# Kernel optimization log

Hardware: AMD Instinct MI355X
Metric: run time of the kernel (lower is better)

The kernel has to match this reference:

```python
import jax, jax.numpy as jnp
import numpy as np

B, S, E, H = 16, 512, 768, 12
D = E // H
SCALING = 1.0 / np.sqrt(D * 1.0)  # scaling_factor = 1


def setup_inputs() -> dict:
    key = jax.random.key(0)
    ks = jax.random.split(key, 8)
    query = jax.random.normal(ks[0], (B, S, E), dtype=jnp.float32)
    key_in = jax.random.normal(ks[1], (B, S, E), dtype=jnp.float32)
    value = jax.random.normal(ks[2], (B, S, E), dtype=jnp.float32)
    key_padding_mask = jax.random.randint(ks[3], (B, S), 0, 2).astype(jnp.bool_)
    attn_bias = jax.random.normal(ks[4], (B, H, S, S), dtype=jnp.float32)
    # Learned params. NOTE: original code applies wq to q, k AND v (wk/wv unused).
    Wq = jax.random.normal(ks[5], (E, E), dtype=jnp.float32) * (1.0 / np.sqrt(E))
    bq = jnp.zeros((E,), dtype=jnp.float32)
    Wo = jax.random.normal(ks[6], (E, E), dtype=jnp.float32) * (1.0 / np.sqrt(E))
    bo = jnp.zeros((E,), dtype=jnp.float32)
    return {"query": query, "key": key_in, "value": value,
            "key_padding_mask": key_padding_mask, "attn_bias": attn_bias,
            "Wq": Wq, "bq": bq, "Wo": Wo, "bo": bo}


def _split_heads(x):
    # [B,S,E] -> [B,H,S,D]
    return x.reshape(B, S, H, D).transpose(0, 2, 1, 3)


def reference(query, key, value, key_padding_mask, attn_bias, Wq, bq, Wo, bo):
    q = (query @ Wq + bq) * jnp.asarray(SCALING, query.dtype)
    k = key @ Wq + bq      # faithful: wq used for k and v in the source
    v = value @ Wq + bq
    q, k, v = _split_heads(q), _split_heads(k), _split_heads(v)  # [B,H,S,D]
    w = jnp.einsum('bhtd,bhsd->bhts', q, k)                      # [B,H,T,S]
    w = jnp.where(key_padding_mask[:, None, None, :], -jnp.inf, w)
    w = w + attn_bias
    attn = jax.nn.softmax(w, axis=-1)  # dropout is no-op (training=False)
    o = jnp.einsum('bhts,bhsd->bhtd', attn, v)
    o = o.transpose(0, 2, 1, 3).reshape(B, S, E)
    o = o @ Wo + bo
    attn_weights = w.reshape(B * H, S, S)
    return (o, attn_weights, attn.reshape(B * H, S, S))
```

## Files before the change

### kernel.cpp

```cpp
#include <hip/hip_runtime.h>
#include <cmath>

#define BB 16
#define SS 512
#define EE 768
#define HH 12
#define DD 64
#define NBH (BB*HH)

#define MASK_NEG (-1.0e30f)

__device__ __forceinline__ unsigned short bf16_rn(float x) {
    unsigned u = __float_as_uint(x);
    u += 0x7FFFu + ((u >> 16) & 1u);
    return (unsigned short)(u >> 16);
}
__device__ __forceinline__ float bf16_tof(unsigned short h) {
    return __uint_as_float(((unsigned)h) << 16);
}

typedef __attribute__((ext_vector_type(8))) short bf16x8;
typedef __attribute__((ext_vector_type(4))) float f32x4;
typedef __attribute__((ext_vector_type(4))) unsigned short u16x4;

__global__ __launch_bounds__(256) void conv_w_kernel(
    const float* __restrict__ Wq, const float* __restrict__ Wo,
    unsigned short* __restrict__ wtq, unsigned short* __restrict__ wto)
{
    const float* __restrict__ W = blockIdx.z ? Wo : Wq;
    unsigned short* __restrict__ wt = blockIdx.z ? wto : wtq;
    const int k = blockIdx.x * 256 + threadIdx.x;
    const int n = blockIdx.y;
    const float x = W[(size_t)k * EE + n];
    const unsigned short h = bf16_rn(x);
    const float r = x - bf16_tof(h);
    const unsigned short m = bf16_rn(r);
    const float l2 = r - bf16_tof(m);
    const unsigned short l = bf16_rn(l2);
    const size_t PL = (size_t)EE * EE;
    wt[0 * PL + (size_t)n * EE + k] = h;
    wt[1 * PL + (size_t)n * EE + k] = m;
    wt[2 * PL + (size_t)n * EE + k] = l;
}

__global__ __launch_bounds__(256) void split_gemm_qkv_kernel(
    const float* __restrict__ Xq, const float* __restrict__ Xk,
    const float* __restrict__ Xv, const unsigned short* __restrict__ wt,
    const float* __restrict__ bvec,
    unsigned short* __restrict__ qp, unsigned short* __restrict__ kp,
    unsigned short* __restrict__ vtp)
{
    const int p = blockIdx.x;
    const int z = p / 384;
    const int q = p % 384;
    const int xcd = q & 7, idx = q >> 3;
    const int m0 = (xcd * 8 + (idx & 7)) * 128;
    const int n0 = (idx >> 3) * 128;

    const float* __restrict__ X = (z == 1) ? Xk : (z == 2) ? Xv : Xq;
    const float scale = (z == 0) ? 0.125f : 1.0f;

    __shared__ __align__(16) unsigned short lds[4 * 4096];
    const int AH = 0, AL = 4096, BH = 8192, BL = 12288;

    const int tid = threadIdx.x;
    const int srow = tid >> 2;
    const int sg   = tid & 3;
    const int wv = tid >> 6;
    const int wr = wv >> 1, wc = wv & 1;
    const int lane = tid & 63;
    const int l15 = lane & 15, lg = lane >> 4;

    const size_t PL = (size_t)EE * EE;
    const size_t PS = (size_t)NBH * SS * DD;

    f32x4 acc[4][4];
#pragma unroll
    for (int i = 0; i < 4; ++i)
#pragma unroll
        for (int j = 0; j < 4; ++j) acc[i][j] = (f32x4){0.f, 0.f, 0.f, 0.f};

    float4 xf[2][2];
    bf16x8 wh[2], wl[2];

#define QKV_LOAD(K0)                                                          \
    {                                                                         \
        _Pragma("unroll")                                                     \
        for (int half = 0; half < 2; ++half) {                                \
            const int row = srow + 64 * half;                                 \
            const float* xp = &X[(size_t)(m0 + row) * EE + (K0) + sg * 8];    \
            xf[half][0] = *reinterpret_cast<const float4*>(xp);               \
            xf[half][1] = *reinterpret_cast<const float4*>(xp + 4);           \
            const size_t bo = (size_t)(n0 + row) * EE + (K0) + sg * 8;        \
            wh[half] = *reinterpret_cast<const bf16x8*>(&wt[0 * PL + bo]);    \
            wl[half] = *reinterpret_cast<const bf16x8*>(&wt[1 * PL + bo]);    \
        }                                                                     \
    }

    QKV_LOAD(0);

#pragma unroll 1
    for (int k0 = 0; k0 < EE; k0 += 32) {
        __syncthreads();
#pragma unroll
        for (int half = 0; half < 2; ++half) {
            const int row = srow + 64 * half;
            const float xs[8] = {xf[half][0].x, xf[half][0].y, xf[half][0].z, xf[half][0].w,
                                 xf[half][1].x, xf[half][1].y, xf[half][1].z, xf[half][1].w};
            bf16x8 hv, mv;
#pragma unroll
            for (int e = 0; e < 8; ++e) {
                const float x = xs[e];
                const unsigned short h = bf16_rn(x);
                const unsigned short m = bf16_rn(x - bf16_tof(h));
                hv[e] = (short)h;
                mv[e] = (short)m;
            }
            const int o = row * 32 + sg * 8;
            *reinterpret_cast<bf16x8*>(&lds[AH + o]) = hv;
            *reinterpret_cast<bf16x8*>(&lds[AL + o]) = mv;
            *reinterpret_cast<bf16x8*>(&lds[BH + o]) = wh[half];
            *reinterpret_cast<bf16x8*>(&lds[BL + o]) = wl[half];
        }
        __syncthreads();

        if (k0 + 32 < EE) QKV_LOAD(k0 + 32);

        bf16x8 ah[4], al[4];
#pragma unroll
        for (int i = 0; i < 4; ++i) {
            const int o = (wr * 64 + i * 16 + l15) * 32 + lg * 8;
            ah[i] = *reinterpret_cast<const bf16x8*>(&lds[AH + o]);
            al[i] = *reinterpret_cast<const bf16x8*>(&lds[AL + o]);
        }
#pragma unroll
        for (int j = 0; j < 4; ++j) {
            const int o = (wc * 64 + j * 16 + l15) * 32 + lg * 8;
            const bf16x8 bh = *reinterpret_cast<const bf16x8*>(&lds[BH + o]);
            const bf16x8 bl = *reinterpret_cast<const bf16x8*>(&lds[BL + o]);
#pragma unroll
            for (int i = 0; i < 4; ++i) {
                acc[i][j] = __builtin_amdgcn_mfma_f32_16x16x32_bf16(ah[i], bh, acc[i][j], 0, 0, 0);
                acc[i][j] = __builtin_amdgcn_mfma_f32_16x16x32_bf16(ah[i], bl, acc[i][j], 0, 0, 0);
                acc[i][j] = __builtin_amdgcn_mfma_f32_16x16x32_bf16(al[i], bh, acc[i][j], 0, 0, 0);
                acc[i][j] = __builtin_amdgcn_mfma_f32_16x16x32_bf16(al[i], bl, acc[i][j], 0, 0, 0);
            }
        }
    }
#undef QKV_LOAD

    unsigned short* __restrict__ dstp = (z == 0) ? qp : kp;
#pragma unroll
    for (int j = 0; j < 4; ++j) {
        const int n = n0 + wc * 64 + j * 16 + l15;
        const float bvn = bvec[n];
        const int h = n >> 6, d = n & 63;
#pragma unroll
        for (int i = 0; i < 4; ++i) {
            const int mb = m0 + wr * 64 + i * 16 + lg * 4;
#pragma unroll
            for (int r = 0; r < 4; ++r) {
                const int m = mb + r;
                const int bh_ = (m >> 9) * HH + h;
                const int srow_ = m & 511;
                const float val = (acc[i][j][r] + bvn) * scale;
                const unsigned short hi = bf16_rn(val);
                const unsigned short lo = bf16_rn(val - bf16_tof(hi));
                if (z == 2) {
                    const size_t o = ((size_t)bh_ * DD + d) * SS + srow_;
                    vtp[o] = hi;
                    vtp[o + PS] = lo;
                } else {
                    const size_t o = ((size_t)bh_ * SS + srow_) * DD + d;
                    dstp[o] = hi;
                    dstp[o + PS] = lo;
                }
            }
        }
    }
}

__global__ __launch_bounds__(256) void flash_attn_kernel(
    const unsigned short* __restrict__ qp, const unsigned short* __restrict__ kp,
    const unsigned short* __restrict__ vt, const unsigned char* __restrict__ mask,
    const float* __restrict__ bias, float* __restrict__ wout,
    float* __restrict__ ohb, float* __restrict__ stat_m,
    float* __restrict__ stat_inv)
{
    const int p = blockIdx.x;
    const int g = p >> 3;
    const int bh = (p & 7) * 24 + (g >> 3);
    const int t0 = (g & 7) * 64;
    const int b = bh / HH, h = bh % HH;
    const int tid = threadIdx.x;
    const int wv = tid >> 6;
    const int lane = tid & 63, l15 = lane & 15, lg = lane >> 4;
    const size_t PS = (size_t)NBH * SS * DD;

    __shared__ __align__(16) unsigned short kbuf[2 * 64 * 68];
    __shared__ __align__(16) unsigned short vbuf[2 * 64 * 68];
    __shared__ __align__(16) unsigned short pbuf[4 * 2 * 16 * 68];

    bf16x8 bqh[2], bql[2];
    {
        const unsigned short* qbase = &qp[((size_t)bh * SS + t0 + wv * 16) * DD];
#pragma unroll
        for (int kc = 0; kc < 2; ++kc) {
            const size_t o = (size_t)l15 * DD + kc * 32 + lg * 8;
            bqh[kc] = *reinterpret_cast<const bf16x8*>(&qbase[o]);
            bql[kc] = *reinterpret_cast<const bf16x8*>(&qbase[o + PS]);
        }
    }

    float rm = -3.0e38f, rs = 0.0f;

    f32x4 oac[4];
#pragma unroll
    for (int j = 0; j < 4; ++j) oac[j] = (f32x4){0.f, 0.f, 0.f, 0.f};

    const int t = t0 + wv * 16 + l15;

    const unsigned short* __restrict__ kb0 = &kp[(size_t)bh * SS * DD];
    const unsigned short* __restrict__ vb0 = &vt[(size_t)bh * DD * SS];
    const int srow2 = tid >> 3, sg2 = (tid & 7) * 8;

    bf16x8 krh[2], krl[2], vrh[2], vrl[2];

#define FA_LOADKV(SC)                                                         \
    {                                                                         \
        _Pragma("unroll")                                                     \
        for (int rep = 0; rep < 2; ++rep) {                                   \
            const int row = srow2 + rep * 32;                                 \
            krh[rep] = *reinterpret_cast<const bf16x8*>(                      \
                &kb0[(size_t)((SC) + row) * DD + sg2]);                       \
            krl[rep] = *reinterpret_cast<const bf16x8*>(                      \
                &kb0[(size_t)((SC) + row) * DD + sg2 + PS]);                  \
            vrh[rep] = *reinterpret_cast<const bf16x8*>(                      \
                &vb0[(size_t)row * SS + (SC) + sg2]);                         \
            vrl[rep] = *reinterpret_cast<const bf16x8*>(                      \
                &vb0[(size_t)row * SS + (SC) + sg2 + PS]);                    \
        }                                                                     \
    }

    FA_LOADKV(0);

#pragma unroll 1
    for (int c = 0; c < 8; ++c) {
        const int sc = c * 64;
        __syncthreads();

#pragma unroll
        for (int rep = 0; rep < 2; ++rep) {
            const int row = srow2 + rep * 32;
            *reinterpret_cast<bf16x8*>(&kbuf[row * 68 + sg2]) = krh[rep];
            *reinterpret_cast<bf16x8*>(&kbuf[64 * 68 + row * 68 + sg2]) = krl[rep];
            *reinterpret_cast<bf16x8*>(&vbuf[row * 68 + sg2]) = vrh[rep];
            *reinterpret_cast<bf16x8*>(&vbuf[64 * 68 + row * 68 + sg2]) = vrl[rep];
        }
        __syncthreads();

        if (c < 7) FA_LOADKV(sc + 64);

        float4 bvr[4];
        uchar4 mkr[4];
#pragma unroll
        for (int i = 0; i < 4; ++i) {
            const int s = sc + i * 16 + lg * 4;
            bvr[i] = *reinterpret_cast<const float4*>(&bias[((size_t)bh * SS + t) * SS + s]);
            mkr[i] = *reinterpret_cast<const uchar4*>(&mask[b * SS + s]);
        }

        f32x4 ws[4];
#pragma unroll
        for (int i = 0; i < 4; ++i) ws[i] = (f32x4){0.f, 0.f, 0.f, 0.f};
#pragma unroll
        for (int kc = 0; kc < 2; ++kc) {
#pragma unroll
            for (int i = 0; i < 4; ++i) {
                const int o = (i * 16 + l15) * 68 + kc * 32 + lg * 8;
                const bf16x8 ah = *reinterpret_cast<const bf16x8*>(&kbuf[o]);
                const bf16x8 al = *reinterpret_cast<const bf16x8*>(&kbuf[64 * 68 + o]);
                ws[i] = __builtin_amdgcn_mfma_f32_16x16x32_bf16(ah, bqh[kc], ws[i], 0, 0, 0);
                ws[i] = __builtin_amdgcn_mfma_f32_16x16x32_bf16(ah, bql[kc], ws[i], 0, 0, 0);
                ws[i] = __builtin_amdgcn_mfma_f32_16x16x32_bf16(al, bqh[kc], ws[i], 0, 0, 0);
                ws[i] = __builtin_amdgcn_mfma_f32_16x16x32_bf16(al, bql[kc], ws[i], 0, 0, 0);
            }
        }

        float mx = -3.0e38f;
#pragma unroll
        for (int i = 0; i < 4; ++i) {
            const int s = sc + i * 16 + lg * 4;
            const size_t go = ((size_t)bh * SS + t) * SS + s;
            float4 w4;
            w4.x = mkr[i].x ? MASK_NEG : ws[i][0] + bvr[i].x;
            w4.y = mkr[i].y ? MASK_NEG : ws[i][1] + bvr[i].y;
            w4.z = mkr[i].z ? MASK_NEG : ws[i][2] + bvr[i].z;
            w4.w = mkr[i].w ? MASK_NEG : ws[i][3] + bvr[i].w;
            *reinterpret_cast<float4*>(&wout[go]) = w4;
            ws[i][0] = w4.x; ws[i][1] = w4.y; ws[i][2] = w4.z; ws[i][3] = w4.w;
            mx = fmaxf(mx, fmaxf(fmaxf(w4.x, w4.y), fmaxf(w4.z, w4.w)));
        }
        mx = fmaxf(mx, __shfl_xor(mx, 16));
        mx = fmaxf(mx, __shfl_xor(mx, 32));

        const float m_new = fmaxf(rm, mx);
        float sm = 0.0f;
#pragma unroll
        for (int i = 0; i < 4; ++i)
#pragma unroll
            for (int r = 0; r < 4; ++r) sm += __expf(ws[i][r] - m_new);
        sm += __shfl_xor(sm, 16);
        sm += __shfl_xor(sm, 32);
        const float scl = __expf(rm - m_new);
        rs = rs * scl + sm;
        rm = m_new;

        unsigned short* pw = &pbuf[(wv * 2) * 16 * 68];
#pragma unroll
        for (int i = 0; i < 4; ++i) {
            float4 p4;
            p4.x = __expf(ws[i][0] - m_new);
            p4.y = __expf(ws[i][1] - m_new);
            p4.z = __expf(ws[i][2] - m_new);
            p4.w = __expf(ws[i][3] - m_new);
            u16x4 hv, lv;
            hv.x = bf16_rn(p4.x); lv.x = bf16_rn(p4.x - bf16_tof(hv.x));
            hv.y = bf16_rn(p4.y); lv.y = bf16_rn(p4.y - bf16_tof(hv.y));
            hv.z = bf16_rn(p4.z); lv.z = bf16_rn(p4.z - bf16_tof(hv.z));
            hv.w = bf16_rn(p4.w); lv.w = bf16_rn(p4.w - bf16_tof(hv.w));
            const int po = l15 * 68 + i * 16 + lg * 4;
            *reinterpret_cast<u16x4*>(&pw[po]) = hv;
            *reinterpret_cast<u16x4*>(&pw[16 * 68 + po]) = lv;
        }

        float sclr[4];
#pragma unroll
        for (int r = 0; r < 4; ++r) sclr[r] = __shfl(scl, lg * 4 + r);
#pragma unroll
        for (int j = 0; j < 4; ++j)
#pragma unroll
            for (int r = 0; r < 4; ++r) oac[j][r] *= sclr[r];

#pragma unroll
        for (int kc = 0; kc < 2; ++kc) {
            const int ko = kc * 32 + lg * 8;
            const bf16x8 pah = *reinterpret_cast<const bf16x8*>(&pw[l15 * 68 + ko]);
            const bf16x8 pal = *reinterpret_cast<const bf16x8*>(&pw[16 * 68 + l15 * 68 + ko]);
#pragma unroll
            for (int j = 0; j < 4; ++j) {
                const int o = (j * 16 + l15) * 68 + ko;
                const bf16x8 vh = *reinterpret_cast<const bf16x8*>(&vbuf[o]);
                const bf16x8 vl = *reinterpret_cast<const bf16x8*>(&vbuf[64 * 68 + o]);
                oac[j] = __builtin_amdgcn_mfma_f32_16x16x32_bf16(pah, vh, oac[j], 0, 0, 0);
                oac[j] = __builtin_amdgcn_mfma_f32_16x16x32_bf16(pah, vl, oac[j], 0, 0, 0);
                oac[j] = __builtin_amdgcn_mfma_f32_16x16x32_bf16(pal, vh, oac[j], 0, 0, 0);
                oac[j] = __builtin_amdgcn_mfma_f32_16x16x32_bf16(pal, vl, oac[j], 0, 0, 0);
            }
        }
    }
#undef FA_LOADKV

    const float inv = 1.0f / rs;
    if (lg == 0) {
        stat_m[(size_t)bh * SS + t] = rm;
        stat_inv[(size_t)bh * SS + t] = inv;
    }
    float invr[4];
#pragma unroll
    for (int r = 0; r < 4; ++r) invr[r] = __shfl(inv, lg * 4 + r);
#pragma unroll
    for (int j = 0; j < 4; ++j)
#pragma unroll
        for (int r = 0; r < 4; ++r) {
            const int tr = t0 + wv * 16 + lg * 4 + r;
            ohb[((size_t)b * SS + tr) * EE + h * DD + j * 16 + l15] = oac[j][r] * invr[r];
        }
}

__global__ __launch_bounds__(256) void finish_kernel(
    const float* __restrict__ X, const unsigned short* __restrict__ wt,
    const float* __restrict__ bvec, float* __restrict__ dflat,
    const float* __restrict__ win, const float* __restrict__ stat_m,
    const float* __restrict__ stat_inv, float* __restrict__ attn)
{
    __shared__ __align__(16) unsigned short lds[6 * 4096];

    if (blockIdx.x >= 384) {
        const int nb = gridDim.x - 384;
        const size_t total = (size_t)NBH * SS * (SS / 4);
        for (size_t g = (size_t)(blockIdx.x - 384) * 256 + threadIdx.x; g < total;
             g += (size_t)nb * 256) {
            const size_t row = g >> 7;
            const float m_ = stat_m[row];
            const float iv = stat_inv[row];
            const float4 w4 = reinterpret_cast<const float4*>(win)[g];
            float4 p4;
            p4.x = __expf(w4.x - m_) * iv;
            p4.y = __expf(w4.y - m_) * iv;
            p4.z = __expf(w4.z - m_) * iv;
            p4.w = __expf(w4.w - m_) * iv;
            reinterpret_cast<float4*>(attn)[g] = p4;
        }
        return;
    }

    const int q = blockIdx.x;
    const int xcd = q & 7, idx = q >> 3;
    const int m0 = (xcd * 8 + (idx & 7)) * 128;
    const int n0 = (idx >> 3) * 128;

    const int AH = 0, AM = 4096, AL = 8192, BH = 12288, BM = 16384, BL = 20480;

    const int tid = threadIdx.x;
    const int srow = tid >> 2;
    const int sg   = tid & 3;
    const int wv = tid >> 6;
    const int wr = wv >> 1, wc = wv & 1;
    const int lane = tid & 63;
    const int l15 = lane & 15, lg = lane >> 4;
    const size_t PL = (size_t)EE * EE;

    f32x4 acc[4][4];
#pragma unroll
    for (int i = 0; i < 4; ++i)
#pragma unroll
        for (int j = 0; j < 4; ++j) acc[i][j] = (f32x4){0.f, 0.f, 0.f, 0.f};

#pragma unroll 1
    for (int k0 = 0; k0 < EE; k0 += 32) {
#pragma unroll
        for (int half = 0; half < 2; ++half) {
            const int row = srow + 64 * half;
            const float* xp = &X[(size_t)(m0 + row) * EE + k0 + sg * 8];
            const float4 f0 = *reinterpret_cast<const float4*>(xp);
            const float4 f1 = *reinterpret_cast<const float4*>(xp + 4);
            const float xs[8] = {f0.x, f0.y, f0.z, f0.w, f1.x, f1.y, f1.z, f1.w};
            bf16x8 hv, mv, lv;
#pragma unroll
            for (int e = 0; e < 8; ++e) {
                const float x = xs[e];
                const unsigned short h = bf16_rn(x);
                const float r = x - bf16_tof(h);
                const unsigned short m = bf16_rn(r);
                const float l2 = r - bf16_tof(m);
                hv[e] = (short)h;
                mv[e] = (short)m;
                lv[e] = (short)bf16_rn(l2);
            }
            const int o = row * 32 + sg * 8;
            *reinterpret_cast<bf16x8*>(&lds[AH + o]) = hv;
            *reinterpret_cast<bf16x8*>(&lds[AM + o]) = mv;
            *reinterpret_cast<bf16x8*>(&lds[AL + o]) = lv;

            const size_t bo = (size_t)(n0 + row) * EE + k0 + sg * 8;
            *reinterpret_cast<bf16x8*>(&lds[BH + o]) =
                *reinterpret_cast<const bf16x8*>(&wt[0 * PL + bo]);
            *reinterpret_cast<bf16x8*>(&lds[BM + o]) =
                *reinterpret_cast<const bf16x8*>(&wt[1 * PL + bo]);
            *reinterpret_cast<bf16x8*>(&lds[BL + o]) =
                *reinterpret_cast<const bf16x8*>(&wt[2 * PL + bo]);
        }
        __syncthreads();

        bf16x8 ah[4], am[4], al[4];
#pragma unroll
        for (int i = 0; i < 4; ++i) {
            const int o = (wr * 64 + i * 16 + l15) * 32 + lg * 8;
            ah[i] = *reinterpret_cast<const bf16x8*>(&lds[AH + o]);
            am[i] = *reinterpret_cast<const bf16x8*>(&lds[AM + o]);
            al[i] = *reinterpret_cast<const bf16x8*>(&lds[AL + o]);
        }
#pragma unroll
        for (int j = 0; j < 4; ++j) {
            const int o = (wc * 64 + j * 16 + l15) * 32 + lg * 8;
            const bf16x8 bh = *reinterpret_cast<const bf16x8*>(&lds[BH + o]);
            const bf16x8 bm = *reinterpret_cast<const bf16x8*>(&lds[BM + o]);
            const bf16x8 bl = *reinterpret_cast<const bf16x8*>(&lds[BL + o]);
#pragma unroll
            for (int i = 0; i < 4; ++i) {
                acc[i][j] = __builtin_amdgcn_mfma_f32_16x16x32_bf16(ah[i], bh, acc[i][j], 0, 0, 0);
                acc[i][j] = __builtin_amdgcn_mfma_f32_16x16x32_bf16(ah[i], bm, acc[i][j], 0, 0, 0);
                acc[i][j] = __builtin_amdgcn_mfma_f32_16x16x32_bf16(am[i], bh, acc[i][j], 0, 0, 0);
                acc[i][j] = __builtin_amdgcn_mfma_f32_16x16x32_bf16(ah[i], bl, acc[i][j], 0, 0, 0);
                acc[i][j] = __builtin_amdgcn_mfma_f32_16x16x32_bf16(al[i], bh, acc[i][j], 0, 0, 0);
                acc[i][j] = __builtin_amdgcn_mfma_f32_16x16x32_bf16(am[i], bm, acc[i][j], 0, 0, 0);
            }
        }
        __syncthreads();
    }

#pragma unroll
    for (int j = 0; j < 4; ++j) {
        const int n = n0 + wc * 64 + j * 16 + l15;
        const float bvn = bvec[n];
#pragma unroll
        for (int i = 0; i < 4; ++i) {
            const int mb = m0 + wr * 64 + i * 16 + lg * 4;
#pragma unroll
            for (int r = 0; r < 4; ++r)
                dflat[(size_t)(mb + r) * EE + n] = acc[i][j][r] + bvn;
        }
    }
}

__global__ __launch_bounds__(256) void proj_kernel(
    const float* __restrict__ Xq, const float* __restrict__ Xk,
    const float* __restrict__ Xv, const float* __restrict__ W,
    const float* __restrict__ bvec, float* __restrict__ qb,
    float* __restrict__ kb, float* __restrict__ vb)
{
    const int z = blockIdx.z;
    const float* __restrict__ X = (z == 0) ? Xq : (z == 1) ? Xk : Xv;
    float* __restrict__ Dst = (z == 0) ? qb : (z == 1) ? kb : vb;
    const float scale = (z == 0) ? 0.125f : 1.0f;

    const int m0 = blockIdx.x * 128;
    const int n0 = blockIdx.y * 128;

    __shared__ float As[16][128];
    __shared__ float Bs[16][128];

    const int tid = threadIdx.x;
    const int ty = tid >> 4, tx = tid & 15;

    float acc[8][8];
#pragma unroll
    for (int i = 0; i < 8; ++i)
#pragma unroll
        for (int j = 0; j < 8; ++j) acc[i][j] = 0.0f;

    const int arow = tid >> 1;
    const int ak   = (tid & 1) * 8;
    const int brow = tid >> 4;
    const int bn   = (tid & 15) * 8;

    for (int k0 = 0; k0 < EE; k0 += 16) {
        const float4* ap = reinterpret_cast<const float4*>(&X[(size_t)(m0 + arow) * EE + k0 + ak]);
        float4 a0 = ap[0], a1 = ap[1];
        As[ak + 0][arow] = a0.x; As[ak + 1][arow] = a0.y;
        As[ak + 2][arow] = a0.z; As[ak + 3][arow] = a0.w;
        As[ak + 4][arow] = a1.x; As[ak + 5][arow] = a1.y;
        As[ak + 6][arow] = a1.z; As[ak + 7][arow] = a1.w;

        const float4* bp = reinterpret_cast<const float4*>(&W[(size_t)(k0 + brow) * EE + n0 + bn]);
        float4 b0 = bp[0], b1 = bp[1];
        *reinterpret_cast<float4*>(&Bs[brow][bn])     = b0;
        *reinterpret_cast<float4*>(&Bs[brow][bn + 4]) = b1;
        __syncthreads();

#pragma unroll
        for (int kk = 0; kk < 16; ++kk) {
            float4 aA = *reinterpret_cast<const float4*>(&As[kk][ty * 8]);
            float4 aB = *reinterpret_cast<const float4*>(&As[kk][ty * 8 + 4]);
            float4 bA = *reinterpret_cast<const float4*>(&Bs[kk][tx * 8]);
            float4 bB = *reinterpret_cast<const float4*>(&Bs[kk][tx * 8 + 4]);
            float av[8] = {aA.x, aA.y, aA.z, aA.w, aB.x, aB.y, aB.z, aB.w};
            float bv[8] = {bA.x, bA.y, bA.z, bA.w, bB.x, bB.y, bB.z, bB.w};
#pragma unroll
            for (int i = 0; i < 8; ++i)
#pragma unroll
                for (int j = 0; j < 8; ++j)
                    acc[i][j] = fmaf(av[i], bv[j], acc[i][j]);
        }
        __syncthreads();
    }

    const int nbase = n0 + tx * 8;
    float bq8[8];
    {
        float4 c0 = *reinterpret_cast<const float4*>(&bvec[nbase]);
        float4 c1 = *reinterpret_cast<const float4*>(&bvec[nbase + 4]);
        bq8[0]=c0.x; bq8[1]=c0.y; bq8[2]=c0.z; bq8[3]=c0.w;
        bq8[4]=c1.x; bq8[5]=c1.y; bq8[6]=c1.z; bq8[7]=c1.w;
    }
    const int hh = nbase >> 6;
    const int dd = nbase & 63;
#pragma unroll
    for (int i = 0; i < 8; ++i) {
        const int m = m0 + ty * 8 + i;
        const int bidx = m >> 9;
        const int srow = m & 511;
        float* dst = &Dst[(((size_t)bidx * HH + hh) * SS + srow) * DD + dd];
        float4 v0, v1;
        v0.x = (acc[i][0] + bq8[0]) * scale;
        v0.y = (acc[i][1] + bq8[1]) * scale;
        v0.z = (acc[i][2] + bq8[2]) * scale;
        v0.w = (acc[i][3] + bq8[3]) * scale;
        v1.x = (acc[i][4] + bq8[4]) * scale;
        v1.y = (acc[i][5] + bq8[5]) * scale;
        v1.z = (acc[i][6] + bq8[6]) * scale;
        v1.w = (acc[i][7] + bq8[7]) * scale;
        *reinterpret_cast<float4*>(dst)     = v0;
        *reinterpret_cast<float4*>(dst + 4) = v1;
    }
}

__global__ __launch_bounds__(256) void scores_kernel(
    const float* __restrict__ qb, const float* __restrict__ kb,
    const unsigned char* __restrict__ mask,
    const float* __restrict__ bias, float* __restrict__ wout)
{
    const int bh = blockIdx.z;
    const int b  = bh / HH;
    const int t0 = blockIdx.y * 128;
    const int s0 = blockIdx.x * 128;

    __shared__ float As[16][128];
    __shared__ float Bs[16][128];

    const int tid = threadIdx.x;
    const int ty = tid >> 4, tx = tid & 15;

    float acc[8][8];
#pragma unroll
    for (int i = 0; i < 8; ++i)
#pragma unroll
        for (int j = 0; j < 8; ++j) acc[i][j] = 0.0f;

    const int arow = tid >> 1;
    const int ak   = (tid & 1) * 8;

    const float* __restrict__ qbase = &qb[(size_t)bh * SS * DD];
    const float* __restrict__ kbase = &kb[(size_t)bh * SS * DD];

    for (int k0 = 0; k0 < DD; k0 += 16) {
        const float4* ap = reinterpret_cast<const float4*>(&qbase[(size_t)(t0 + arow) * DD + k0 + ak]);
        float4 a0 = ap[0], a1 = ap[1];
        As[ak + 0][arow] = a0.x; As[ak + 1][arow] = a0.y;
        As[ak + 2][arow] = a0.z; As[ak + 3][arow] = a0.w;
        As[ak + 4][arow] = a1.x; As[ak + 5][arow] = a1.y;
        As[ak + 6][arow] = a1.z; As[ak + 7][arow] = a1.w;

        const float4* bp = reinterpret_cast<const float4*>(&kbase[(size_t)(s0 + arow) * DD + k0 + ak]);
        float4 b0 = bp[0], b1 = bp[1];
        Bs[ak + 0][arow] = b0.x; Bs[ak + 1][arow] = b0.y;
        Bs[ak + 2][arow] = b0.z; Bs[ak + 3][arow] = b0.w;
        Bs[ak + 4][arow] = b1.x; Bs[ak + 5][arow] = b1.y;
        Bs[ak + 6][arow] = b1.z; Bs[ak + 7][arow] = b1.w;
        __syncthreads();

#pragma unroll
        for (int kk = 0; kk < 16; ++kk) {
            float4 aA = *reinterpret_cast<const float4*>(&As[kk][ty * 8]);
            float4 aB = *reinterpret_cast<const float4*>(&As[kk][ty * 8 + 4]);
            float4 bA = *reinterpret_cast<const float4*>(&Bs[kk][tx * 8]);
            float4 bB = *reinterpret_cast<const float4*>(&Bs[kk][tx * 8 + 4]);
            float av[8] = {aA.x, aA.y, aA.z, aA.w, aB.x, aB.y, aB.z, aB.w};
            float bv[8] = {bA.x, bA.y, bA.z, bA.w, bB.x, bB.y, bB.z, bB.w};
#pragma unroll
            for (int i = 0; i < 8; ++i)
#pragma unroll
                for (int j = 0; j < 8; ++j)
                    acc[i][j] = fmaf(av[i], bv[j], acc[i][j]);
        }
        __syncthreads();
    }

    const int scol = s0 + tx * 8;
    const uint2 mv = *reinterpret_cast<const uint2*>(&mask[b * SS + scol]);
    bool msk[8];
    msk[0] = (mv.x & 0x000000ffu) != 0;
    msk[1] = (mv.x & 0x0000ff00u) != 0;
    msk[2] = (mv.x & 0x00ff0000u) != 0;
    msk[3] = (mv.x & 0xff000000u) != 0;
    msk[4] = (mv.y & 0x000000ffu) != 0;
    msk[5] = (mv.y & 0x0000ff00u) != 0;
    msk[6] = (mv.y & 0x00ff0000u) != 0;
    msk[7] = (mv.y & 0xff000000u) != 0;
#pragma unroll
    for (int i = 0; i < 8; ++i) {
        const int t = t0 + ty * 8 + i;
        const float4 bv0 = *reinterpret_cast<const float4*>(&bias[((size_t)bh * SS + t) * SS + scol]);
        const float4 bv1 = *reinterpret_cast<const float4*>(&bias[((size_t)bh * SS + t) * SS + scol + 4]);
        float4 w0, w1;
        w0.x = msk[0] ? MASK_NEG : acc[i][0] + bv0.x;
        w0.y = msk[1] ? MASK_NEG : acc[i][1] + bv0.y;
        w0.z = msk[2] ? MASK_NEG : acc[i][2] + bv0.z;
        w0.w = msk[3] ? MASK_NEG : acc[i][3] + bv0.w;
        w1.x = msk[4] ? MASK_NEG : acc[i][4] + bv1.x;
        w1.y = msk[5] ? MASK_NEG : acc[i][5] + bv1.y;
        w1.z = msk[6] ? MASK_NEG : acc[i][6] + bv1.z;
        w1.w = msk[7] ? MASK_NEG : acc[i][7] + bv1.w;
        float* wrow = &wout[((size_t)bh * SS + t) * SS + scol];
        *reinterpret_cast<float4*>(wrow)     = w0;
        *reinterpret_cast<float4*>(wrow + 4) = w1;
    }
}

__global__ __launch_bounds__(256) void softmax_pv_kernel(
    const float* __restrict__ win, const float* __restrict__ vb,
    float* __restrict__ attn, float* __restrict__ ohb)
{
    const int bh = blockIdx.y;
    const int b = bh / HH, h = bh % HH;
    const int t0 = blockIdx.x * 64;
    const int wave = threadIdx.x >> 6;
    const int lane = threadIdx.x & 63;

    __shared__ float pws[4][8][512];

#pragma unroll 1
    for (int g = 0; g < 2; ++g) {
        const int tb = t0 + wave * 16 + g * 8;

#pragma unroll 1
        for (int r = 0; r < 8; ++r) {
            const int t = tb + r;
            const float4* wp = reinterpret_cast<const float4*>(&win[((size_t)bh * SS + t) * SS + lane * 8]);
            float4 w0 = wp[0], w1 = wp[1];
            float wv[8] = {w0.x,w0.y,w0.z,w0.w,w1.x,w1.y,w1.z,w1.w};
            float mx = wv[0];
#pragma unroll
            for (int j = 1; j < 8; ++j) mx = fmaxf(mx, wv[j]);
#pragma unroll
            for (int off = 32; off > 0; off >>= 1)
                mx = fmaxf(mx, __shfl_xor(mx, off));
            float e[8];
            float sum = 0.0f;
#pragma unroll
            for (int j = 0; j < 8; ++j) { e[j] = __expf(wv[j] - mx); sum += e[j]; }
#pragma unroll
            for (int off = 32; off > 0; off >>= 1)
                sum += __shfl_xor(sum, off);
            const float inv = 1.0f / sum;
            float4 p0, p1;
            p0.x = e[0]*inv; p0.y = e[1]*inv; p0.z = e[2]*inv; p0.w = e[3]*inv;
            p1.x = e[4]*inv; p1.y = e[5]*inv; p1.z = e[6]*inv; p1.w = e[7]*inv;
            float* arow = &attn[((size_t)bh * SS + t) * SS + lane * 8];
            *reinterpret_cast<float4*>(arow)     = p0;
            *reinterpret_cast<float4*>(arow + 4) = p1;
            *reinterpret_cast<float4*>(&pws[wave][r][lane * 8])     = p0;
            *reinterpret_cast<float4*>(&pws[wave][r][lane * 8 + 4]) = p1;
        }
        __syncthreads();

        float oacc[8] = {0,0,0,0,0,0,0,0};
#pragma unroll 2
        for (int s = 0; s < SS; s += 4) {
            const float v0 = vb[((size_t)bh * SS + s + 0) * DD + lane];
            const float v1 = vb[((size_t)bh * SS + s + 1) * DD + lane];
            const float v2 = vb[((size_t)bh * SS + s + 2) * DD + lane];
            const float v3 = vb[((size_t)bh * SS + s + 3) * DD + lane];
#pragma unroll
            for (int r = 0; r < 8; ++r) {
                const float4 p4 = *reinterpret_cast<const float4*>(&pws[wave][r][s]);
                oacc[r] = fmaf(p4.x, v0, oacc[r]);
                oacc[r] = fmaf(p4.y, v1, oacc[r]);
                oacc[r] = fmaf(p4.z, v2, oacc[r]);
                oacc[r] = fmaf(p4.w, v3, oacc[r]);
            }
        }
#pragma unroll
        for (int r = 0; r < 8; ++r)
            ohb[((size_t)b * SS + tb + r) * EE + h * DD + lane] = oacc[r];
        __syncthreads();
    }
}

__global__ __launch_bounds__(256) void outproj_kernel(
    const float* __restrict__ A, const float* __restrict__ W,
    const float* __restrict__ bvec, float* __restrict__ out)
{
    const int m0 = blockIdx.x * 128;
    const int n0 = blockIdx.y * 128;

    __shared__ float As[16][128];
    __shared__ float Bs[16][128];

    const int tid = threadIdx.x;
    const int ty = tid >> 4, tx = tid & 15;

    float acc[8][8];
#pragma unroll
    for (int i = 0; i < 8; ++i)
#pragma unroll
        for (int j = 0; j < 8; ++j) acc[i][j] = 0.0f;

    const int arow = tid >> 1;
    const int ak   = (tid & 1) * 8;
    const int brow = tid >> 4;
    const int bn   = (tid & 15) * 8;

    for (int k0 = 0; k0 < EE; k0 += 16) {
        const float4* ap = reinterpret_cast<const float4*>(&A[(size_t)(m0 + arow) * EE + k0 + ak]);
        float4 a0 = ap[0], a1 = ap[1];
        As[ak + 0][arow] = a0.x; As[ak + 1][arow] = a0.y;
        As[ak + 2][arow] = a0.z; As[ak + 3][arow] = a0.w;
        As[ak + 4][arow] = a1.x; As[ak + 5][arow] = a1.y;
        As[ak + 6][arow] = a1.z; As[ak + 7][arow] = a1.w;

        const float4* bp = reinterpret_cast<const float4*>(&W[(size_t)(k0 + brow) * EE + n0 + bn]);
        float4 b0 = bp[0], b1 = bp[1];
        *reinterpret_cast<float4*>(&Bs[brow][bn])     = b0;
        *reinterpret_cast<float4*>(&Bs[brow][bn + 4]) = b1;
        __syncthreads();

#pragma unroll
        for (int kk = 0; kk < 16; ++kk) {
            float4 aA = *reinterpret_cast<const float4*>(&As[kk][ty * 8]);
            float4 aB = *reinterpret_cast<const float4*>(&As[kk][ty * 8 + 4]);
            float4 bA = *reinterpret_cast<const float4*>(&Bs[kk][tx * 8]);
            float4 bB = *reinterpret_cast<const float4*>(&Bs[kk][tx * 8 + 4]);
            float av[8] = {aA.x, aA.y, aA.z, aA.w, aB.x, aB.y, aB.z, aB.w};
            float bv[8] = {bA.x, bA.y, bA.z, bA.w, bB.x, bB.y, bB.z, bB.w};
#pragma unroll
            for (int i = 0; i < 8; ++i)
#pragma unroll
                for (int j = 0; j < 8; ++j)
                    acc[i][j] = fmaf(av[i], bv[j], acc[i][j]);
        }
        __syncthreads();
    }

    const int nbase = n0 + tx * 8;
    float bq8[8];
    {
        float4 c0 = *reinterpret_cast<const float4*>(&bvec[nbase]);
        float4 c1 = *reinterpret_cast<const float4*>(&bvec[nbase + 4]);
        bq8[0]=c0.x; bq8[1]=c0.y; bq8[2]=c0.z; bq8[3]=c0.w;
        bq8[4]=c1.x; bq8[5]=c1.y; bq8[6]=c1.z; bq8[7]=c1.w;
    }
#pragma unroll
    for (int i = 0; i < 8; ++i) {
        const int m = m0 + ty * 8 + i;
        float* dst = &out[(size_t)m * EE + nbase];
        float4 v0, v1;
        v0.x = acc[i][0] + bq8[0]; v0.y = acc[i][1] + bq8[1];
        v0.z = acc[i][2] + bq8[2]; v0.w = acc[i][3] + bq8[3];
        v1.x = acc[i][4] + bq8[4]; v1.y = acc[i][5] + bq8[5];
        v1.z = acc[i][6] + bq8[6]; v1.w = acc[i][7] + bq8[7];
        *reinterpret_cast<float4*>(dst)     = v0;
        *reinterpret_cast<float4*>(dst + 4) = v1;
    }
}

extern "C" void kernel_launch(void* const* d_in, const int* in_sizes, int n_in,
                              void* d_out, int out_size, void* d_ws, size_t ws_size,
                              hipStream_t stream)
{
    const float* query = (const float*)d_in[0];
    const float* key   = (const float*)d_in[1];
    const float* value = (const float*)d_in[2];
    const unsigned char* mask = (const unsigned char*)d_in[3];
    const float* bias  = (const float*)d_in[4];
    const float* Wq    = (const float*)d_in[5];
    const float* bq    = (const float*)d_in[6];
    const float* Wo    = (const float*)d_in[7];
    const float* bo    = (const float*)d_in[8];

    float* out_o = (float*)d_out;
    float* out_w = out_o + (size_t)BB * SS * EE;
    float* out_a = out_w + (size_t)NBH * SS * SS;

    const size_t headsz = (size_t)NBH * SS * DD;
    const size_t wt_elems = 3 * (size_t)EE * EE;

    const size_t need_mfma = 3 * (2 * headsz * sizeof(unsigned short))
                           + headsz * sizeof(float)
                           + 2 * wt_elems * sizeof(unsigned short);

    if (ws_size >= need_mfma) {
        unsigned short* qp = (unsigned short*)d_ws;
        unsigned short* kp = qp + 2 * headsz;
        unsigned short* vt = kp + 2 * headsz;
        float* ohb = (float*)(vt + 2 * headsz);
        unsigned short* wtq = (unsigned short*)(ohb + headsz);
        unsigned short* wto = wtq + wt_elems;
        float* stat_m   = (float*)wtq;
        float* stat_inv = stat_m + (size_t)NBH * SS;

        conv_w_kernel<<<dim3(3, EE, 2), 256, 0, stream>>>(Wq, Wo, wtq, wto);
        split_gemm_qkv_kernel<<<dim3(3 * 384), 256, 0, stream>>>(
            query, key, value, wtq, bq, qp, kp, vt);
        flash_attn_kernel<<<dim3(8 * NBH), 256, 0, stream>>>(
            qp, kp, vt, mask, bias, out_w, ohb, stat_m, stat_inv);
        finish_kernel<<<384 + 2048, 256, 0, stream>>>(
            ohb, wto, bo, out_o, out_w, stat_m, stat_inv, out_a);
    } else {
        const size_t base_bytes = 4 * headsz * sizeof(float);
        if (ws_size < base_bytes) return;
        float* qb  = (float*)d_ws;
        float* kb  = qb + headsz;
        float* vb  = kb + headsz;
        float* ohb = vb + headsz;
        proj_kernel<<<dim3(64, 6, 3), 256, 0, stream>>>(query, key, value, Wq, bq, qb, kb, vb);
        scores_kernel<<<dim3(4, 4, NBH), 256, 0, stream>>>(qb, kb, mask, bias, out_w);
        softmax_pv_kernel<<<dim3(8, NBH), 256, 0, stream>>>(out_w, vb, out_a, ohb);
        outproj_kernel<<<dim3(64, 6), 256, 0, stream>>>(ohb, Wo, bo, out_o);
    }
}
```

Before: 430.7 us.

## Load K/V MFMA fragments directly from global memory, dropping LDS staging

The flash-attention kernel no longer stages K and V tiles through shared memory with register double-buffering and two block barriers per chunk. Each wave now reads its MFMA operand fragments straight from global memory, relying on L1/L2 caching for reuse across the four waves. This removes the LDS traffic and __syncthreads stalls, at the cost of redundant global loads per wave and losing the software prefetch overlap. Load latency is now exposed right before the MFMAs.

```diff
diff --git a/kernel.cpp b/kernel.cpp
--- a/kernel.cpp
+++ b/kernel.cpp
@@ -197,8 +197,6 @@
     const int lane = tid & 63, l15 = lane & 15, lg = lane >> 4;
     const size_t PS = (size_t)NBH * SS * DD;
 
-    __shared__ __align__(16) unsigned short kbuf[2 * 64 * 68];
-    __shared__ __align__(16) unsigned short vbuf[2 * 64 * 68];
     __shared__ __align__(16) unsigned short pbuf[4 * 2 * 16 * 68];
 
     bf16x8 bqh[2], bql[2];
@@ -222,44 +220,11 @@
 
     const unsigned short* __restrict__ kb0 = &kp[(size_t)bh * SS * DD];
     const unsigned short* __restrict__ vb0 = &vt[(size_t)bh * DD * SS];
-    const int srow2 = tid >> 3, sg2 = (tid & 7) * 8;
-
-    bf16x8 krh[2], krl[2], vrh[2], vrl[2];
-
-#define FA_LOADKV(SC)                                                         \
-    {                                                                         \
-        _Pragma("unroll")                                                     \
-        for (int rep = 0; rep < 2; ++rep) {                                   \
-            const int row = srow2 + rep * 32;                                 \
-            krh[rep] = *reinterpret_cast<const bf16x8*>(                      \
-                &kb0[(size_t)((SC) + row) * DD + sg2]);                       \
-            krl[rep] = *reinterpret_cast<const bf16x8*>(                      \
-                &kb0[(size_t)((SC) + row) * DD + sg2 + PS]);                  \
-            vrh[rep] = *reinterpret_cast<const bf16x8*>(                      \
-                &vb0[(size_t)row * SS + (SC) + sg2]);                         \
-            vrl[rep] = *reinterpret_cast<const bf16x8*>(                      \
-                &vb0[(size_t)row * SS + (SC) + sg2 + PS]);                    \
-        }                                                                     \
-    }
-
-    FA_LOADKV(0);
+    unsigned short* pw = &pbuf[(wv * 2) * 16 * 68];
 
 #pragma unroll 1
     for (int c = 0; c < 8; ++c) {
         const int sc = c * 64;
-        __syncthreads();
-
-#pragma unroll
-        for (int rep = 0; rep < 2; ++rep) {
-            const int row = srow2 + rep * 32;
-            *reinterpret_cast<bf16x8*>(&kbuf[row * 68 + sg2]) = krh[rep];
-            *reinterpret_cast<bf16x8*>(&kbuf[64 * 68 + row * 68 + sg2]) = krl[rep];
-            *reinterpret_cast<bf16x8*>(&vbuf[row * 68 + sg2]) = vrh[rep];
-            *reinterpret_cast<bf16x8*>(&vbuf[64 * 68 + row * 68 + sg2]) = vrl[rep];
-        }
-        __syncthreads();
-
-        if (c < 7) FA_LOADKV(sc + 64);
 
         float4 bvr[4];
         uchar4 mkr[4];
@@ -275,15 +240,19 @@
         for (int i = 0; i < 4; ++i) ws[i] = (f32x4){0.f, 0.f, 0.f, 0.f};
 #pragma unroll
         for (int kc = 0; kc < 2; ++kc) {
+            bf16x8 ah[4], al[4];
 #pragma unroll
             for (int i = 0; i < 4; ++i) {
-                const int o = (i * 16 + l15) * 68 + kc * 32 + lg * 8;
-                const bf16x8 ah = *reinterpret_cast<const bf16x8*>(&kbuf[o]);
-                const bf16x8 al = *reinterpret_cast<const bf16x8*>(&kbuf[64 * 68 + o]);
-                ws[i] = __builtin_amdgcn_mfma_f32_16x16x32_bf16(ah, bqh[kc], ws[i], 0, 0, 0);
-                ws[i] = __builtin_amdgcn_mfma_f32_16x16x32_bf16(ah, bql[kc], ws[i], 0, 0, 0);
-                ws[i] = __builtin_amdgcn_mfma_f32_16x16x32_bf16(al, bqh[kc], ws[i], 0, 0, 0);
-                ws[i] = __builtin_amdgcn_mfma_f32_16x16x32_bf16(al, bql[kc], ws[i], 0, 0, 0);
+                const size_t ko = (size_t)(sc + i * 16 + l15) * DD + kc * 32 + lg * 8;
+                ah[i] = *reinterpret_cast<const bf16x8*>(&kb0[ko]);
+                al[i] = *reinterpret_cast<const bf16x8*>(&kb0[ko + PS]);
+            }
+#pragma unroll
+            for (int i = 0; i < 4; ++i) {
+                ws[i] = __builtin_amdgcn_mfma_f32_16x16x32_bf16(ah[i], bqh[kc], ws[i], 0, 0, 0);
+                ws[i] = __builtin_amdgcn_mfma_f32_16x16x32_bf16(ah[i], bql[kc], ws[i], 0, 0, 0);
+                ws[i] = __builtin_amdgcn_mfma_f32_16x16x32_bf16(al[i], bqh[kc], ws[i], 0, 0, 0);
+                ws[i] = __builtin_amdgcn_mfma_f32_16x16x32_bf16(al[i], bql[kc], ws[i], 0, 0, 0);
             }
         }
 
@@ -316,7 +285,6 @@
         rs = rs * scl + sm;
         rm = m_new;
 
-        unsigned short* pw = &pbuf[(wv * 2) * 16 * 68];
 #pragma unroll
         for (int i = 0; i < 4; ++i) {
             float4 p4;
@@ -349,9 +317,9 @@
             const bf16x8 pal = *reinterpret_cast<const bf16x8*>(&pw[16 * 68 + l15 * 68 + ko]);
 #pragma unroll
             for (int j = 0; j < 4; ++j) {
-                const int o = (j * 16 + l15) * 68 + ko;
-                const bf16x8 vh = *reinterpret_cast<const bf16x8*>(&vbuf[o]);
-                const bf16x8 vl = *reinterpret_cast<const bf16x8*>(&vbuf[64 * 68 + o]);
+                const size_t vo = (size_t)(j * 16 + l15) * SS + sc + ko;
+                const bf16x8 vh = *reinterpret_cast<const bf16x8*>(&vb0[vo]);
+                const bf16x8 vl = *reinterpret_cast<const bf16x8*>(&vb0[vo + PS]);
                 oac[j] = __builtin_amdgcn_mfma_f32_16x16x32_bf16(pah, vh, oac[j], 0, 0, 0);
                 oac[j] = __builtin_amdgcn_mfma_f32_16x16x32_bf16(pah, vl, oac[j], 0, 0, 0);
                 oac[j] = __builtin_amdgcn_mfma_f32_16x16x32_bf16(pal, vh, oac[j], 0, 0, 0);
@@ -359,7 +327,6 @@
             }
         }
     }
-#undef FA_LOADKV
 
     const float inv = 1.0f / rs;
     if (lg == 0) {
```

New measurement: 542.1 us. 1.26x slower.
